# Performance work log

Measured on AMD Instinct MI355X. Metric: run time of the kernel, lower is better.

Reference implementation:

```python
import jax, jax.numpy as jnp
import numpy as np

D_MODEL = 1024
N_HEADS = 16
HEAD_DIM = D_MODEL // N_HEADS
D_FF = 4096
LN_EPS = 1e-5


def setup_inputs() -> dict:
    key = jax.random.key(0)
    ks = jax.random.split(key, 13)
    s = lambda fan_in: 1.0 / np.sqrt(fan_in)
    return {
        "x": jax.random.normal(ks[0], (2, 2048, D_MODEL), dtype=jnp.float32),
        "w_qkv": jax.random.uniform(ks[1], (D_MODEL, 3 * D_MODEL), jnp.float32, -s(D_MODEL), s(D_MODEL)),
        "b_qkv": jax.random.uniform(ks[2], (3 * D_MODEL,), jnp.float32, -s(D_MODEL), s(D_MODEL)),
        "w_out": jax.random.uniform(ks[3], (D_MODEL, D_MODEL), jnp.float32, -s(D_MODEL), s(D_MODEL)),
        "b_out": jax.random.uniform(ks[4], (D_MODEL,), jnp.float32, -s(D_MODEL), s(D_MODEL)),
        "w_ff1": jax.random.uniform(ks[5], (D_MODEL, D_FF), jnp.float32, -s(D_MODEL), s(D_MODEL)),
        "b_ff1": jax.random.uniform(ks[6], (D_FF,), jnp.float32, -s(D_MODEL), s(D_MODEL)),
        "w_ff2": jax.random.uniform(ks[7], (D_FF, D_MODEL), jnp.float32, -s(D_FF), s(D_FF)),
        "b_ff2": jax.random.uniform(ks[8], (D_MODEL,), jnp.float32, -s(D_FF), s(D_FF)),
        "ln1_g": jnp.ones((D_MODEL,), jnp.float32),
        "ln1_b": jnp.zeros((D_MODEL,), jnp.float32),
        "ln2_g": jnp.ones((D_MODEL,), jnp.float32),
        "ln2_b": jnp.zeros((D_MODEL,), jnp.float32),
    }


def _layer_norm(x, g, b):
    mu = jnp.mean(x, axis=-1, keepdims=True)
    var = jnp.mean(jnp.square(x - mu), axis=-1, keepdims=True)
    return (x - mu) * jax.lax.rsqrt(var + LN_EPS) * g + b


def reference(x, w_qkv, b_qkv, w_out, b_out, w_ff1, b_ff1, w_ff2, b_ff2,
              ln1_g, ln1_b, ln2_g, ln2_b):
    B, S, D = x.shape
    scale = HEAD_DIM ** -0.5
    qkv = x @ w_qkv + b_qkv                                   # [B,S,3D]
    qkv = qkv.reshape(B, S, 3, N_HEADS, HEAD_DIM)
    q, k, v = (qkv[:, :, 0], qkv[:, :, 1], qkv[:, :, 2])      # [B,S,H,Dh]
    attn = jnp.einsum("bqhd,bkhd->bhqk", q, k) * scale        # [B,H,S,S]
    attn = jax.nn.softmax(attn, axis=-1)
    o = jnp.einsum("bhqk,bkhd->bqhd", attn, v).reshape(B, S, D)
    o = o @ w_out + b_out
    x = _layer_norm(x + o, ln1_g, ln1_b)
    # FFN: Linear -> exact GELU -> Linear (dropout = 0)
    h = jax.nn.gelu(x @ w_ff1 + b_ff1, approximate=False)
    ff = h @ w_ff2 + b_ff2
    x = _layer_norm(x + ff, ln2_g, ln2_b)
    return x
```

## Files before the change

kernel.cpp:

```cpp
#include <hip/hip_runtime.h>
#include <hip/hip_bf16.h>
#include <cstdint>
#include <cstddef>

using bf16 = __hip_bfloat16;
typedef __attribute__((ext_vector_type(8))) short bf16x8;
typedef __attribute__((ext_vector_type(4))) float f32x4;

#define TOKENS 4096
#define DMODEL 1024
#define DFF    4096
#define SEQ    2048
#define NHEAD  16
#define HDIM   64
#define KVBLK  64
#define NT     (SEQ / KVBLK)

__device__ __forceinline__ void async16(const void* g, void* l) {
  __builtin_amdgcn_global_load_lds(
      (const __attribute__((address_space(1))) void*)g,
      (__attribute__((address_space(3))) void*)l, 16, 0, 0);
}

__device__ __forceinline__ f32x4 mfma16(bf16x8 a, bf16x8 b, f32x4 c) {
  return __builtin_amdgcn_mfma_f32_16x16x32_bf16(a, b, c, 0, 0, 0);
}

__global__ void cast_bf16_k(const float* __restrict__ src, bf16* __restrict__ dst, int n) {
  int i = (blockIdx.x * blockDim.x + threadIdx.x) * 4;
  if (i >= n) return;
  float4 v = *(const float4*)(src + i);
  dst[i + 0] = __float2bfloat16(v.x);
  dst[i + 1] = __float2bfloat16(v.y);
  dst[i + 2] = __float2bfloat16(v.z);
  dst[i + 3] = __float2bfloat16(v.w);
}

__global__ void transpose_cast_k(const float* __restrict__ src, bf16* __restrict__ dst,
                                 int K, int N) {
  __shared__ float tile[32][33];
  int nt = blockIdx.x * 32, kt = blockIdx.y * 32;
  int tx = threadIdx.x, ty = threadIdx.y;
  #pragma unroll
  for (int i = 0; i < 32; i += 8)
    tile[ty + i][tx] = src[(size_t)(kt + ty + i) * N + nt + tx];
  __syncthreads();
  #pragma unroll
  for (int i = 0; i < 32; i += 8)
    dst[(size_t)(nt + ty + i) * K + kt + tx] = __float2bfloat16(tile[tx][ty + i]);
}

template <int EPI>
__global__ __launch_bounds__(256, 2)
void gemm_bt(const bf16* __restrict__ A, const bf16* __restrict__ Bt,
             const float* __restrict__ bias, int M, int N, int K,
             float* __restrict__ outf, bf16* __restrict__ outb,
             const float* __restrict__ resid,
             bf16* __restrict__ Qb, bf16* __restrict__ Kb, bf16* __restrict__ Vtb) {
  __shared__ bf16 Al[128 * 32];
  __shared__ bf16 Bl[128 * 32];
  const int t = threadIdx.x;
  const int nwg = gridDim.x * gridDim.y;
  const int flat = blockIdx.y * gridDim.x + blockIdx.x;
  const int swz = (flat & 7) * (nwg >> 3) + (flat >> 3);
  const int bm = (swz / gridDim.x) * 128, bn = (swz % gridDim.x) * 128;
  const int wid = t >> 6, lane = t & 63, g = lane >> 4, r = lane & 15;
  const int wr = (wid >> 1) * 64, wc = (wid & 1) * 64;

  const f32x4 zero = {0.f, 0.f, 0.f, 0.f};
  f32x4 acc[4][4];
  #pragma unroll
  for (int i = 0; i < 4; i++)
    #pragma unroll
    for (int j = 0; j < 4; j++) acc[i][j] = zero;

  const int ch0 = t, ch1 = t + 256;
  const int r0 = ch0 >> 2, c0 = (ch0 & 3) * 8;
  const int r1 = ch1 >> 2, c1 = (ch1 & 3) * 8;

  #pragma unroll 1
  for (int kt = 0; kt < K; kt += 32) {
    async16(A + (size_t)(bm + r0) * K + kt + c0, (char*)Al + ch0 * 16);
    async16(A + (size_t)(bm + r1) * K + kt + c1, (char*)Al + ch1 * 16);
    async16(Bt + (size_t)(bn + r0) * K + kt + c0, (char*)Bl + ch0 * 16);
    async16(Bt + (size_t)(bn + r1) * K + kt + c1, (char*)Bl + ch1 * 16);
    __syncthreads();
    bf16x8 af[4], bfr[4];
    #pragma unroll
    for (int mt = 0; mt < 4; mt++) af[mt] = *(const bf16x8*)&Al[(wr + mt * 16 + r) * 32 + 8 * g];
    #pragma unroll
    for (int nt = 0; nt < 4; nt++) bfr[nt] = *(const bf16x8*)&Bl[(wc + nt * 16 + r) * 32 + 8 * g];
    #pragma unroll
    for (int mt = 0; mt < 4; mt++)
      #pragma unroll
      for (int nt = 0; nt < 4; nt++)
        acc[mt][nt] = mfma16(af[mt], bfr[nt], acc[mt][nt]);
    __syncthreads();
  }

  #pragma unroll
  for (int nt = 0; nt < 4; nt++) {
    const int col = bn + wc + nt * 16 + r;
    const float bv = bias[col];
    #pragma unroll
    for (int mt = 0; mt < 4; mt++) {
      #pragma unroll
      for (int j = 0; j < 4; j++) {
        const int row = bm + wr + mt * 16 + 4 * g + j;
        float v = acc[mt][nt][j] + bv;
        if constexpr (EPI == 0) {
          const int part = col >> 10, hd = col & 1023, h = hd >> 6, d = hd & 63;
          const int b_ = row >> 11, s_ = row & 2047;
          const bf16 q = __float2bfloat16(v);
          if (part == 0)      Qb[((size_t)(b_ * NHEAD + h) * SEQ + s_) * HDIM + d] = q;
          else if (part == 1) Kb[((size_t)(b_ * NHEAD + h) * SEQ + s_) * HDIM + d] = q;
          else                Vtb[((size_t)(b_ * NHEAD + h) * HDIM + d) * SEQ + s_] = q;
        } else if constexpr (EPI == 1) {
          const size_t idx = (size_t)row * N + col;
          outf[idx] = v + resid[idx];
        } else {
          const size_t idx = (size_t)row * N + col;
          outb[idx] = __float2bfloat16(0.5f * v * (1.f + erff(v * 0.70710678118f)));
        }
      }
    }
  }
}

__global__ __launch_bounds__(256, 4)
void attn_k(const bf16* __restrict__ Q, const bf16* __restrict__ Km,
            const bf16* __restrict__ Vt, bf16* __restrict__ O) {
  __shared__ bf16 Kl[2][KVBLK * 64];
  __shared__ bf16 Vl[2][KVBLK * 64];
  __shared__ bf16 P[4][16 * 64];
  const int b = blockIdx.x;
  const int bswz = (b & 7) * 128 + (b >> 3);
  const int bh = bswz >> 5, qb = bswz & 31;
  const int t = threadIdx.x, wid = t >> 6, lane = t & 63, g = lane >> 4, r = lane & 15;
  const int q0 = qb * 64 + wid * 16;
  const bf16* Qp = Q + (size_t)bh * SEQ * HDIM;
  const char* Kc = (const char*)(Km + (size_t)bh * SEQ * HDIM);
  const char* Vc = (const char*)(Vt + (size_t)bh * HDIM * SEQ);

  const bf16x8 qf0 = *(const bf16x8*)&Qp[(q0 + r) * HDIM + 8 * g];
  const bf16x8 qf1 = *(const bf16x8*)&Qp[(q0 + r) * HDIM + 8 * g + 32];

  const int o0 = wid * 2048 + lane * 16, o1 = o0 + 1024;
  const int cs0 = ((((o0 >> 4) & 7) ^ ((o0 >> 7) & 7)) << 4);
  const int cs1 = ((((o1 >> 4) & 7) ^ ((o1 >> 7) & 7)) << 4);
  const int kso0 = (o0 & ~127) + cs0, kso1 = (o1 & ~127) + cs1;
  const int vso0 = (o0 >> 7) * (SEQ * 2) + cs0, vso1 = (o1 >> 7) * (SEQ * 2) + cs1;

  const f32x4 zero = {0.f, 0.f, 0.f, 0.f};
  f32x4 oacc[4];
  #pragma unroll
  for (int i = 0; i < 4; i++) oacc[i] = zero;
  float mrow = -1e30f, lrow = 0.f;
  bf16* pl = P[wid];
  const int cA = ((g ^ (r & 7)) << 3), cB = (((g + 4) ^ (r & 7)) << 3);

  {
    const char* ks = Kc; const char* vs = Vc;
    char* kd = (char*)Kl[0]; char* vd = (char*)Vl[0];
    async16(ks + kso0, kd + o0); async16(ks + kso1, kd + o1);
    async16(vs + vso0, vd + o0); async16(vs + vso1, vd + o1);
  }

  #pragma unroll 1
  for (int tt = 0; tt < NT; ++tt) {
    if (tt + 1 < NT) {
      const char* ks = Kc + (tt + 1) * (KVBLK * HDIM * 2);
      const char* vs = Vc + (tt + 1) * (KVBLK * 2);
      char* kd = (char*)Kl[(tt + 1) & 1]; char* vd = (char*)Vl[(tt + 1) & 1];
      async16(ks + kso0, kd + o0); async16(ks + kso1, kd + o1);
      async16(vs + vso0, vd + o0); async16(vs + vso1, vd + o1);
      asm volatile("s_waitcnt vmcnt(4)" ::: "memory");
    } else {
      asm volatile("s_waitcnt vmcnt(0)" ::: "memory");
    }
    __builtin_amdgcn_sched_barrier(0);
    __builtin_amdgcn_s_barrier();
    __builtin_amdgcn_sched_barrier(0);

    const bf16* kbuf = Kl[tt & 1];
    const bf16* vbuf = Vl[tt & 1];

    f32x4 sacc[4];
    #pragma unroll
    for (int kt = 0; kt < 4; kt++) {
      const bf16* krow = kbuf + (kt * 16 + r) * 64;
      bf16x8 ka = *(const bf16x8*)&krow[cA];
      bf16x8 kb = *(const bf16x8*)&krow[cB];
      f32x4 s = zero;
      s = mfma16(ka, qf0, s);
      s = mfma16(kb, qf1, s);
      sacc[kt] = s;
    }

    float sv[4][4];
    #pragma unroll
    for (int kt = 0; kt < 4; kt++)
      #pragma unroll
      for (int j = 0; j < 4; j++) sv[kt][j] = sacc[kt][j] * 0.125f;
    float m0 = fmaxf(fmaxf(sv[0][0], sv[0][1]), fmaxf(sv[0][2], sv[0][3]));
    float m1 = fmaxf(fmaxf(sv[1][0], sv[1][1]), fmaxf(sv[1][2], sv[1][3]));
    float m2 = fmaxf(fmaxf(sv[2][0], sv[2][1]), fmaxf(sv[2][2], sv[2][3]));
    float m3 = fmaxf(fmaxf(sv[3][0], sv[3][1]), fmaxf(sv[3][2], sv[3][3]));
    float mx = fmaxf(fmaxf(m0, m1), fmaxf(m2, m3));
    mx = fmaxf(mx, __shfl_xor(mx, 16));
    mx = fmaxf(mx, __shfl_xor(mx, 32));
    const float mn = fmaxf(mrow, mx);
    const float corr = __expf(mrow - mn);
    mrow = mn;
    float sum = 0.f;
    #pragma unroll
    for (int kt = 0; kt < 4; kt++)
      #pragma unroll
      for (int j = 0; j < 4; j++) {
        const float p = __expf(sv[kt][j] - mn);
        sv[kt][j] = p;
        sum += p;
      }
    sum += __shfl_xor(sum, 16);
    sum += __shfl_xor(sum, 32);
    lrow = lrow * corr + sum;

    #pragma unroll
    for (int kt = 0; kt < 4; kt++) {
      bf16 pk[4] = {__float2bfloat16(sv[kt][0]), __float2bfloat16(sv[kt][1]),
                    __float2bfloat16(sv[kt][2]), __float2bfloat16(sv[kt][3])};
      const int pc = (((kt * 2 + (g >> 1)) ^ (r & 7)) << 4) + ((g & 1) << 3);
      *(short4*)((char*)pl + r * 128 + pc) = *(const short4*)pk;
    }
    asm volatile("s_waitcnt lgkmcnt(0)" ::: "memory");
    __builtin_amdgcn_sched_barrier(0);
    const bf16x8 pf0 = *(const bf16x8*)((const char*)pl + r * 128 + (cA << 1));
    const bf16x8 pf1 = *(const bf16x8*)((const char*)pl + r * 128 + (cB << 1));

    float cq[4];
    #pragma unroll
    for (int j = 0; j < 4; j++) cq[j] = __shfl(corr, 4 * g + j);

    #pragma unroll
    for (int dt = 0; dt < 4; dt++) {
      const bf16* vrow = vbuf + (dt * 16 + r) * 64;
      bf16x8 v0 = *(const bf16x8*)&vrow[cA];
      bf16x8 v1 = *(const bf16x8*)&vrow[cB];
      #pragma unroll
      for (int j = 0; j < 4; j++) oacc[dt][j] *= cq[j];
      oacc[dt] = mfma16(pf0, v0, oacc[dt]);
      oacc[dt] = mfma16(pf1, v1, oacc[dt]);
    }
    __builtin_amdgcn_sched_barrier(0);
    __builtin_amdgcn_s_barrier();
  }

  float lq[4];
  #pragma unroll
  for (int j = 0; j < 4; j++) lq[j] = __shfl(lrow, 4 * g + j);
  const int b_ = bh >> 4, h = bh & 15;
  #pragma unroll
  for (int dt = 0; dt < 4; dt++)
    #pragma unroll
    for (int j = 0; j < 4; j++) {
      const int tok = b_ * SEQ + q0 + 4 * g + j;
      O[(size_t)tok * DMODEL + h * HDIM + dt * 16 + r] =
          __float2bfloat16(oacc[dt][j] / lq[j]);
    }
}

__global__ __launch_bounds__(256)
void ln_k(const float* __restrict__ in, const float* __restrict__ gw,
          const float* __restrict__ bw, float* __restrict__ outf,
          bf16* __restrict__ outb) {
  const int row = blockIdx.x, t = threadIdx.x;
  const float4 v = *(const float4*)(in + (size_t)row * DMODEL + t * 4);
  float s = v.x + v.y + v.z + v.w;
  float s2 = v.x * v.x + v.y * v.y + v.z * v.z + v.w * v.w;
  #pragma unroll
  for (int m = 1; m < 64; m <<= 1) { s += __shfl_xor(s, m); s2 += __shfl_xor(s2, m); }
  __shared__ float red[8];
  const int wid = t >> 6, lane = t & 63;
  if (lane == 0) { red[wid] = s; red[4 + wid] = s2; }
  __syncthreads();
  s = red[0] + red[1] + red[2] + red[3];
  s2 = red[4] + red[5] + red[6] + red[7];
  const float mu = s * (1.f / DMODEL);
  const float rstd = rsqrtf(s2 * (1.f / DMODEL) - mu * mu + 1e-5f);
  const float4 gv = *(const float4*)(gw + t * 4);
  const float4 bv = *(const float4*)(bw + t * 4);
  float o0 = (v.x - mu) * rstd * gv.x + bv.x;
  float o1 = (v.y - mu) * rstd * gv.y + bv.y;
  float o2 = (v.z - mu) * rstd * gv.z + bv.z;
  float o3 = (v.w - mu) * rstd * gv.w + bv.w;
  if (outf) {
    float4 ov = {o0, o1, o2, o3};
    *(float4*)(outf + (size_t)row * DMODEL + t * 4) = ov;
  }
  if (outb) {
    bf16* p = outb + (size_t)row * DMODEL + t * 4;
    p[0] = __float2bfloat16(o0); p[1] = __float2bfloat16(o1);
    p[2] = __float2bfloat16(o2); p[3] = __float2bfloat16(o3);
  }
}

extern "C" void kernel_launch(void* const* d_in, const int* in_sizes, int n_in,
                              void* d_out, int out_size, void* d_ws, size_t ws_size,
                              hipStream_t stream) {
  const float* x     = (const float*)d_in[0];
  const float* w_qkv = (const float*)d_in[1];
  const float* b_qkv = (const float*)d_in[2];
  const float* w_out = (const float*)d_in[3];
  const float* b_out = (const float*)d_in[4];
  const float* w_ff1 = (const float*)d_in[5];
  const float* b_ff1 = (const float*)d_in[6];
  const float* w_ff2 = (const float*)d_in[7];
  const float* b_ff2 = (const float*)d_in[8];
  const float* ln1_g = (const float*)d_in[9];
  const float* ln1_b = (const float*)d_in[10];
  const float* ln2_g = (const float*)d_in[11];
  const float* ln2_b = (const float*)d_in[12];
  float* out = (float*)d_out;

  char* base = (char*)d_ws;
  bf16* wqkvT = (bf16*)(base);
  bf16* woutT = (bf16*)(base + 6291456);
  bf16* wff1T = (bf16*)(base + 8388608);
  bf16* wff2T = (bf16*)(base + 16777216);
  bf16* Qb    = (bf16*)(base + 25165824);
  bf16* Kb    = (bf16*)(base + 33554432);
  bf16* Vtb   = (bf16*)(base + 41943040);
  bf16* xob   = (bf16*)(base + 50331648);
  bf16* hb    = (bf16*)(base + 25165824);
  float* y    = (float*)(base + 58720256);
  float* x1f  = (float*)(base + 75497472);
  bf16* x1b   = (bf16*)(base + 92274688);
  (void)in_sizes; (void)n_in; (void)out_size; (void)ws_size;

  dim3 tb(32, 8);
  transpose_cast_k<<<dim3(3072 / 32, 1024 / 32), tb, 0, stream>>>(w_qkv, wqkvT, 1024, 3072);
  transpose_cast_k<<<dim3(1024 / 32, 1024 / 32), tb, 0, stream>>>(w_out, woutT, 1024, 1024);
  transpose_cast_k<<<dim3(4096 / 32, 1024 / 32), tb, 0, stream>>>(w_ff1, wff1T, 1024, 4096);
  transpose_cast_k<<<dim3(1024 / 32, 4096 / 32), tb, 0, stream>>>(w_ff2, wff2T, 4096, 1024);
  cast_bf16_k<<<(TOKENS * DMODEL / 4 + 255) / 256, 256, 0, stream>>>(x, xob, TOKENS * DMODEL);

  gemm_bt<0><<<dim3(3072 / 128, TOKENS / 128), 256, 0, stream>>>(
      xob, wqkvT, b_qkv, TOKENS, 3072, 1024, nullptr, nullptr, nullptr, Qb, Kb, Vtb);
  attn_k<<<dim3(1024), 256, 0, stream>>>(Qb, Kb, Vtb, xob);
  gemm_bt<1><<<dim3(1024 / 128, TOKENS / 128), 256, 0, stream>>>(
      xob, woutT, b_out, TOKENS, 1024, 1024, y, nullptr, x, nullptr, nullptr, nullptr);
  ln_k<<<TOKENS, 256, 0, stream>>>(y, ln1_g, ln1_b, x1f, x1b);
  gemm_bt<2><<<dim3(4096 / 128, TOKENS / 128), 256, 0, stream>>>(
      x1b, wff1T, b_ff1, TOKENS, 4096, 1024, nullptr, hb, nullptr, nullptr, nullptr, nullptr);
  gemm_bt<1><<<dim3(1024 / 128, TOKENS / 128), 256, 0, stream>>>(
      hb, wff2T, b_ff2, TOKENS, 1024, 4096, y, nullptr, x1f, nullptr, nullptr, nullptr);
  ln_k<<<TOKENS, 256, 0, stream>>>(y, ln2_g, ln2_b, out, nullptr);
}
```

Baseline: 312.2 us.

## Double-buffer GEMM LDS tiles and use 128x64 tiles for N=1024 GEMMs

The GEMM main loop now double-buffers the A/B LDS tiles, prefetching the next K-tile with async global-to-LDS loads while MFMAs run on the current one. Each iteration needs a single waitcnt plus barrier instead of two syncthreads. A BN template parameter adds a 128x64 tile variant, used for the two N=1024 GEMMs (out-projection and FF2) to double their workgroup count and fill more CUs. This costs twice the LDS per block and gives less reuse per tile in the narrow variant.

Result: faster. 290.7 us (-6.9%).

```diff
diff --git a/kernel.cpp b/kernel.cpp
--- a/kernel.cpp
+++ b/kernel.cpp
@@ -50,60 +50,79 @@
     dst[(size_t)(nt + ty + i) * K + kt + tx] = __float2bfloat16(tile[tx][ty + i]);
 }
 
-template <int EPI>
+template <int EPI, int BN>
 __global__ __launch_bounds__(256, 2)
 void gemm_bt(const bf16* __restrict__ A, const bf16* __restrict__ Bt,
              const float* __restrict__ bias, int M, int N, int K,
              float* __restrict__ outf, bf16* __restrict__ outb,
              const float* __restrict__ resid,
              bf16* __restrict__ Qb, bf16* __restrict__ Kb, bf16* __restrict__ Vtb) {
-  __shared__ bf16 Al[128 * 32];
-  __shared__ bf16 Bl[128 * 32];
+  constexpr int MR = (BN == 128) ? 4 : 2;
+  __shared__ bf16 Al[2][128 * 32];
+  __shared__ bf16 Bl[2][BN * 32];
   const int t = threadIdx.x;
   const int nwg = gridDim.x * gridDim.y;
   const int flat = blockIdx.y * gridDim.x + blockIdx.x;
   const int swz = (flat & 7) * (nwg >> 3) + (flat >> 3);
-  const int bm = (swz / gridDim.x) * 128, bn = (swz % gridDim.x) * 128;
+  const int bm = (swz / gridDim.x) * 128, bn = (swz % gridDim.x) * BN;
   const int wid = t >> 6, lane = t & 63, g = lane >> 4, r = lane & 15;
-  const int wr = (wid >> 1) * 64, wc = (wid & 1) * 64;
+  const int wr = (BN == 128) ? (wid >> 1) * 64 : wid * 32;
+  const int wc = (BN == 128) ? (wid & 1) * 64 : 0;
 
   const f32x4 zero = {0.f, 0.f, 0.f, 0.f};
-  f32x4 acc[4][4];
-  #pragma unroll
-  for (int i = 0; i < 4; i++)
+  f32x4 acc[MR][4];
+  #pragma unroll
+  for (int i = 0; i < MR; i++)
     #pragma unroll
     for (int j = 0; j < 4; j++) acc[i][j] = zero;
 
-  const int ch0 = t, ch1 = t + 256;
-  const int r0 = ch0 >> 2, c0 = (ch0 & 3) * 8;
-  const int r1 = ch1 >> 2, c1 = (ch1 & 3) * 8;
+  const int ar0 = t >> 2, ac = (t & 3) * 8;
+  const int ar1 = ar0 + 64;
+  const int ach0 = t * 16, ach1 = ach0 + 4096;
+
+  const int NK = K >> 5;
+  #define STAGE(ktile, pb)                                                          \
+    do {                                                                            \
+      const int kk = (ktile) << 5;                                                  \
+      async16(A + (size_t)(bm + ar0) * K + kk + ac, (char*)Al[pb] + ach0);          \
+      async16(A + (size_t)(bm + ar1) * K + kk + ac, (char*)Al[pb] + ach1);          \
+      async16(Bt + (size_t)(bn + ar0) * K + kk + ac, (char*)Bl[pb] + ach0);         \
+      if constexpr (BN == 128)                                                      \
+        async16(Bt + (size_t)(bn + ar1) * K + kk + ac, (char*)Bl[pb] + ach1);       \
+    } while (0)
+
+  STAGE(0, 0);
+  asm volatile("s_waitcnt vmcnt(0)" ::: "memory");
+  __builtin_amdgcn_s_barrier();
 
   #pragma unroll 1
-  for (int kt = 0; kt < K; kt += 32) {
-    async16(A + (size_t)(bm + r0) * K + kt + c0, (char*)Al + ch0 * 16);
-    async16(A + (size_t)(bm + r1) * K + kt + c1, (char*)Al + ch1 * 16);
-    async16(Bt + (size_t)(bn + r0) * K + kt + c0, (char*)Bl + ch0 * 16);
-    async16(Bt + (size_t)(bn + r1) * K + kt + c1, (char*)Bl + ch1 * 16);
-    __syncthreads();
-    bf16x8 af[4], bfr[4];
-    #pragma unroll
-    for (int mt = 0; mt < 4; mt++) af[mt] = *(const bf16x8*)&Al[(wr + mt * 16 + r) * 32 + 8 * g];
-    #pragma unroll
-    for (int nt = 0; nt < 4; nt++) bfr[nt] = *(const bf16x8*)&Bl[(wc + nt * 16 + r) * 32 + 8 * g];
-    #pragma unroll
-    for (int mt = 0; mt < 4; mt++)
+  for (int it = 0; it < NK; ++it) {
+    const int cur = it & 1;
+    if (it + 1 < NK) STAGE(it + 1, cur ^ 1);
+    bf16x8 af[MR], bfr[4];
+    #pragma unroll
+    for (int mt = 0; mt < MR; mt++)
+      af[mt] = *(const bf16x8*)&Al[cur][(wr + mt * 16 + r) * 32 + 8 * g];
+    #pragma unroll
+    for (int nt = 0; nt < 4; nt++)
+      bfr[nt] = *(const bf16x8*)&Bl[cur][(wc + nt * 16 + r) * 32 + 8 * g];
+    #pragma unroll
+    for (int mt = 0; mt < MR; mt++)
       #pragma unroll
       for (int nt = 0; nt < 4; nt++)
         acc[mt][nt] = mfma16(af[mt], bfr[nt], acc[mt][nt]);
-    __syncthreads();
-  }
+    __builtin_amdgcn_sched_barrier(0);
+    asm volatile("s_waitcnt vmcnt(0)" ::: "memory");
+    __builtin_amdgcn_s_barrier();
+  }
+  #undef STAGE
 
   #pragma unroll
   for (int nt = 0; nt < 4; nt++) {
     const int col = bn + wc + nt * 16 + r;
     const float bv = bias[col];
     #pragma unroll
-    for (int mt = 0; mt < 4; mt++) {
+    for (int mt = 0; mt < MR; mt++) {
       #pragma unroll
       for (int j = 0; j < 4; j++) {
         const int row = bm + wr + mt * 16 + 4 * g + j;
@@ -344,15 +363,15 @@
   transpose_cast_k<<<dim3(1024 / 32, 4096 / 32), tb, 0, stream>>>(w_ff2, wff2T, 4096, 1024);
   cast_bf16_k<<<(TOKENS * DMODEL / 4 + 255) / 256, 256, 0, stream>>>(x, xob, TOKENS * DMODEL);
 
-  gemm_bt<0><<<dim3(3072 / 128, TOKENS / 128), 256, 0, stream>>>(
+  gemm_bt<0, 128><<<dim3(3072 / 128, TOKENS / 128), 256, 0, stream>>>(
       xob, wqkvT, b_qkv, TOKENS, 3072, 1024, nullptr, nullptr, nullptr, Qb, Kb, Vtb);
   attn_k<<<dim3(1024), 256, 0, stream>>>(Qb, Kb, Vtb, xob);
-  gemm_bt<1><<<dim3(1024 / 128, TOKENS / 128), 256, 0, stream>>>(
+  gemm_bt<1, 64><<<dim3(1024 / 64, TOKENS / 128), 256, 0, stream>>>(
       xob, woutT, b_out, TOKENS, 1024, 1024, y, nullptr, x, nullptr, nullptr, nullptr);
   ln_k<<<TOKENS, 256, 0, stream>>>(y, ln1_g, ln1_b, x1f, x1b);
-  gemm_bt<2><<<dim3(4096 / 128, TOKENS / 128), 256, 0, stream>>>(
+  gemm_bt<2, 128><<<dim3(4096 / 128, TOKENS / 128), 256, 0, stream>>>(
       x1b, wff1T, b_ff1, TOKENS, 4096, 1024, nullptr, hb, nullptr, nullptr, nullptr, nullptr);
-  gemm_bt<1><<<dim3(1024 / 128, TOKENS / 128), 256, 0, stream>>>(
+  gemm_bt<1, 64><<<dim3(1024 / 64, TOKENS / 128), 256, 0, stream>>>(
       hb, wff2T, b_ff2, TOKENS, 1024, 4096, y, nullptr, x1f, nullptr, nullptr, nullptr);
   ln_k<<<TOKENS, 256, 0, stream>>>(y, ln2_g, ln2_b, out, nullptr);
 }
```
